# Optimization experiments

Hardware: AMD Instinct MI355X
Metric: run time of the kernel (lower is better)

## Reference

```python
import jax, jax.numpy as jnp
import numpy as np

DIM = 256
QK = 256
HEADS = 8
NWIN = 16
TOPK = 4
MLP_RATIO = 4
SCALE = QK ** -0.5


def setup_inputs() -> dict:
    key = jax.random.key(0)
    ks = jax.random.split(key, 8)
    p = lambda k, shp: jax.random.normal(k, shp, jnp.float32) * 0.02
    hid = MLP_RATIO * DIM
    return {
        "x": jax.random.normal(ks[0], (8, DIM, 64, 64), jnp.float32),
        # to_q / to_kv : 1x1 Conv2d_BN (eval-mode BN with running stats 0/1 -> scale+shift)
        "wq": p(ks[1], (QK, DIM)), "gq": jnp.ones((QK,), jnp.float32), "bq": jnp.zeros((QK,), jnp.float32),
        "wkv": p(ks[2], (QK + DIM, DIM)), "gkv": jnp.ones((QK + DIM,), jnp.float32), "bkv": jnp.zeros((QK + DIM,), jnp.float32),
        # LEPE depthwise 5x5 conv
        "w_lepe": p(ks[3], (DIM, 1, 5, 5)), "b_lepe": jnp.zeros((DIM,), jnp.float32),
        # Mlp: fc1(1x1 Conv2d_BN) -> dwconv3x3 -> ReLU -> fc2(1x1 Conv2d_BN)
        "w_fc1": p(ks[4], (hid, DIM)), "g_fc1": jnp.ones((hid,), jnp.float32), "b_fc1": jnp.zeros((hid,), jnp.float32),
        "w_dw": p(ks[5], (hid, 1, 3, 3)), "b_dw": jnp.zeros((hid,), jnp.float32),
        "w_fc2": p(ks[6], (DIM, hid)), "g_fc2": jnp.ones((DIM,), jnp.float32), "b_fc2": jnp.zeros((DIM,), jnp.float32),
    }


def _dwconv(x, w, b, pad):
    # x: NCHW, w: (C,1,k,k) depthwise
    out = jax.lax.conv_general_dilated(
        x, w, (1, 1), [(pad, pad), (pad, pad)],
        feature_group_count=x.shape[1],
        dimension_numbers=("NCHW", "OIHW", "NCHW"))
    return out + b[None, :, None, None]


def _bra(x, wq, gq, bq, wkv, gkv, bkv, w_lepe, b_lepe):
    # Bi-Level Routing Attention. x: NCHW
    N, C, H, W = x.shape
    j = i = NWIN
    h, w_ = H // j, W // i          # per-window spatial (4,4)
    p2, w2 = j * i, h * w_          # 256 windows, 16 tokens/window
    xh = x.transpose(0, 2, 3, 1)    # NHWC
    # windowize: (N, p2, h, w, C)
    xw = xh.reshape(N, j, h, i, w_, C).transpose(0, 1, 3, 2, 4, 5).reshape(N, p2, h, w_, C)
    # 1x1 conv + BN(eval: stats 0/1) == matmul * gamma + beta
    q = (xw @ wq.T) * gq + bq                    # (N,p2,h,w,QK)
    kv = (xw @ wkv.T) * gkv + bkv                # (N,p2,h,w,QK+C)
    q_pix = q.reshape(N, p2, w2, QK)
    kv_pix = kv.reshape(N, p2, w2, QK + C)       # identity kv_down
    q_win = q.mean((2, 3))                       # (N,p2,QK)
    k_win = kv[..., :QK].mean((2, 3))            # (N,p2,QK)
    # LEPE on V in full-image layout
    v_img = kv[..., QK:].reshape(N, j, i, h, w_, C).transpose(0, 1, 3, 2, 4, 5).reshape(N, H, W, C)
    lepe = _dwconv(v_img.transpose(0, 3, 1, 2), w_lepe, b_lepe, 2).transpose(0, 2, 3, 1)  # NHWC
    # window-level topk routing (detached, non-differentiable)
    qd = jax.lax.stop_gradient(q_win)
    kd = jax.lax.stop_gradient(k_win)
    logit = (qd * SCALE) @ kd.transpose(0, 2, 1)            # (N,p2,p2)
    _, r_idx = jax.lax.top_k(logit, TOPK)                   # (N,p2,TOPK); r_weight unused (mul_weight='none')
    # gather selected KV windows: (N,p2,TOPK,w2,QK+C)
    kv_sel = jax.vmap(lambda kvp, idx: kvp[idx])(kv_pix, r_idx)
    ch_k, ch_v = QK // HEADS, C // HEADS
    k_sel = kv_sel[..., :QK].reshape(N, p2, TOPK * w2, HEADS, ch_k).transpose(0, 1, 3, 2, 4)
    v_sel = kv_sel[..., QK:].reshape(N, p2, TOPK * w2, HEADS, ch_v).transpose(0, 1, 3, 2, 4)
    qh = q_pix.reshape(N, p2, w2, HEADS, ch_k).transpose(0, 1, 3, 2, 4)
    attn = jax.nn.softmax(jnp.einsum("npmqc,npmkc->npmqk", qh * SCALE, k_sel), axis=-1)
    out = jnp.einsum("npmqk,npmkc->npmqc", attn, v_sel)     # (N,p2,HEADS,w2,ch_v)
    out = out.transpose(0, 1, 3, 2, 4).reshape(N, j, i, h, w_, C)
    out = out.transpose(0, 1, 3, 2, 4, 5).reshape(N, H, W, C)
    out = out + lepe                                         # wo = Identity
    return out.transpose(0, 3, 1, 2)                         # NCHW


def reference(x, wq, gq, bq, wkv, gkv, bkv, w_lepe, b_lepe,
              w_fc1, g_fc1, b_fc1, w_dw, b_dw, w_fc2, g_fc2, b_fc2):
    # top_Block: x = x + attn(x); x = x + mlp(x)   (drop_path inactive in eval)
    x = x + _bra(x, wq, gq, bq, wkv, gkv, bkv, w_lepe, b_lepe)
    h1 = jnp.einsum("nchw,dc->ndhw", x, w_fc1) * g_fc1[None, :, None, None] + b_fc1[None, :, None, None]
    h1 = jax.nn.relu(_dwconv(h1, w_dw, b_dw, 1))
    h2 = jnp.einsum("nchw,dc->ndhw", h1, w_fc2) * g_fc2[None, :, None, None] + b_fc2[None, :, None, None]
    return x + h2
```

## Files before the change

kernel.cpp:

```cpp
#include <hip/hip_runtime.h>
#include <hip/hip_bf16.h>

#define NBATCH 8
#define CDIM 256
#define HH 64
#define WW 64
#define HWSZ 4096
#define TT 32768
#define QKVD 768
#define TOPK 4
#define HID 1024
#define ATTN_SCALE 0.0625f

typedef __hip_bfloat16 bf16;
typedef __attribute__((ext_vector_type(8))) short s8v;
typedef __attribute__((ext_vector_type(4))) float f4v;

__device__ __forceinline__ float toF(bf16 v) { return __bfloat162float(v); }
__device__ __forceinline__ bf16  toB(float v) { return __float2bfloat16(v); }

__global__ void k_prep(const float* __restrict__ wq, const float* __restrict__ gq,
                       const float* __restrict__ wkv, const float* __restrict__ gkv,
                       const float* __restrict__ wfc1, const float* __restrict__ gfc1,
                       const float* __restrict__ wfc2, const float* __restrict__ gfc2,
                       const float* __restrict__ bq, const float* __restrict__ bkv,
                       const float* __restrict__ w_dw, const float* __restrict__ b_dw,
                       bf16* __restrict__ wbqkv, bf16* __restrict__ wbfc1,
                       bf16* __restrict__ wbfc2, float* __restrict__ bias768,
                       float* __restrict__ wdwT) {
    int i = blockIdx.x * 256 + threadIdx.x;
    if (i < 196608) {
        int r = i >> 8;
        float g = (r < 256) ? gq[r] : gkv[r - 256];
        float w = (r < 256) ? wq[i] : wkv[i - 65536];
        wbqkv[i] = toB(w * g);
        if (i < 768) bias768[i] = (i < 256) ? bq[i] : bkv[i - 256];
    } else if (i < 458752) {
        int j = i - 196608;
        wbfc1[j] = toB(wfc1[j] * gfc1[j >> 8]);
    } else if (i < 720896) {
        int j = i - 458752;
        wbfc2[j] = toB(wfc2[j] * gfc2[j >> 10]);
    } else if (i < 731136) {
        int j = i - 720896;
        int cg = j / 80, r = j - cg * 80;
        wdwT[j] = (r < 72) ? w_dw[(cg * 8 + r / 9) * 9 + (r % 9)]
                           : b_dw[cg * 8 + (r - 72)];
    }
}

__global__ void k_xt(const float* __restrict__ x, bf16* __restrict__ xt) {
    __shared__ float tile[32][33];
    int s0 = blockIdx.x * 32, c0 = blockIdx.y * 32, n = blockIdx.z;
    int tx = threadIdx.x, ty = threadIdx.y;
#pragma unroll
    for (int r = 0; r < 4; r++)
        tile[ty + r * 8][tx] = x[(size_t)n * CDIM * HWSZ + (size_t)(c0 + ty + r * 8) * HWSZ + s0 + tx];
    __syncthreads();
#pragma unroll
    for (int r = 0; r < 4; r++)
        xt[((size_t)n * HWSZ + s0 + ty + r * 8) * CDIM + c0 + tx] = toB(tile[tx][ty + r * 8]);
}

__global__ void k_xwin(const float* __restrict__ x, float* __restrict__ xwin) {
    int b = blockIdx.x;
    int n = b >> 8, c = b & 255;
    int p = threadIdx.x, wy = p >> 4, wx = p & 15;
    const float* pl = x + ((size_t)n * CDIM + c) * HWSZ;
    float s = 0.f;
#pragma unroll
    for (int dy = 0; dy < 4; dy++)
#pragma unroll
        for (int dx = 0; dx < 4; dx++)
            s += pl[(wy * 4 + dy) * WW + wx * 4 + dx];
    xwin[((size_t)(n << 8) + p) * 256 + c] = s * 0.0625f;
}

__global__ void k_qkwin(const float* __restrict__ xwin,
                        const float* __restrict__ wq, const float* __restrict__ wkv,
                        const float* __restrict__ gq, const float* __restrict__ bq,
                        const float* __restrict__ gkv, const float* __restrict__ bkv,
                        float* __restrict__ qkwin) {
    __shared__ float As[16][68];
    __shared__ float Bs[16][68];
    int m0 = blockIdx.x * 64, n0 = blockIdx.y * 64;
    int tid = threadIdx.x;
    int tx = tid & 15, ty = tid >> 4;
    float acc[4][4] = {};
    for (int k0 = 0; k0 < 256; k0 += 16) {
#pragma unroll
        for (int r = 0; r < 4; r++) {
            int lin = tid + r * 256;
            int row = lin >> 4, kk = lin & 15;
            As[kk][row] = xwin[(size_t)(m0 + row) * 256 + k0 + kk];
            int n = n0 + row;
            const float* wr = (n < 256) ? (wq + (size_t)n * 256) : (wkv + (size_t)(n - 256) * 256);
            Bs[kk][row] = wr[k0 + kk];
        }
        __syncthreads();
#pragma unroll
        for (int kk = 0; kk < 16; kk++) {
            float a[4], bb[4];
#pragma unroll
            for (int i = 0; i < 4; i++) a[i] = As[kk][tx * 4 + i];
#pragma unroll
            for (int j = 0; j < 4; j++) bb[j] = Bs[kk][ty * 4 + j];
#pragma unroll
            for (int i = 0; i < 4; i++)
#pragma unroll
                for (int j = 0; j < 4; j++) acc[i][j] += a[i] * bb[j];
        }
        __syncthreads();
    }
#pragma unroll
    for (int j = 0; j < 4; j++) {
        int n = n0 + ty * 4 + j;
        float gg = (n < 256) ? gq[n] : gkv[n - 256];
        float bb = (n < 256) ? bq[n] : bkv[n - 256];
#pragma unroll
        for (int i = 0; i < 4; i++)
            qkwin[(size_t)(m0 + tx * 4 + i) * 512 + n] = acc[i][j] * gg + bb;
    }
}

__global__ void k_route(const float* __restrict__ qkwin, int* __restrict__ topk) {
    __shared__ float qrow[256];
    __shared__ float vals[256];
    __shared__ float rv[256];
    __shared__ int ri[256];
    int b = blockIdx.x;
    int n = b >> 8, pq = b & 255;
    int tid = threadIdx.x;
    qrow[tid] = qkwin[((size_t)(n << 8) + pq) * 512 + tid];
    __syncthreads();
    const float* krow = qkwin + ((size_t)(n << 8) + tid) * 512 + 256;
    float dot = 0.f;
    for (int o = 0; o < 256; o++) dot += qrow[o] * krow[o];
    vals[tid] = dot;
    __syncthreads();
    for (int sel = 0; sel < TOPK; sel++) {
        rv[tid] = vals[tid];
        ri[tid] = tid;
        __syncthreads();
        for (int off = 128; off > 0; off >>= 1) {
            if (tid < off) {
                if (rv[tid + off] > rv[tid] ||
                    (rv[tid + off] == rv[tid] && ri[tid + off] < ri[tid])) {
                    rv[tid] = rv[tid + off];
                    ri[tid] = ri[tid + off];
                }
            }
            __syncthreads();
        }
        if (tid == 0) {
            topk[((size_t)(n << 8) + pq) * TOPK + sel] = ri[0];
            vals[ri[0]] = -INFINITY;
        }
        __syncthreads();
    }
}

template <int BM, int BN, int OUTMODE>
__global__ __launch_bounds__(256) void k_mfma(const bf16* __restrict__ A,
                                              const bf16* __restrict__ Wb,
                                              const float* __restrict__ bias,
                                              bf16* __restrict__ out,
                                              bf16* __restrict__ out2,
                                              int M, int N, int K) {
    constexpr int WROWS = BM / 2, WCOLS = BN / 2;
    constexpr int WM = WROWS / 16, WN = WCOLS / 16;
    constexpr int CA = (BM * 4) / 256;
    constexpr int CB = (BN * 4) / 256;
    __shared__ bf16 As[BM * 32];
    __shared__ bf16 Bs[BN * 32];
    int m0 = blockIdx.x * BM, n0 = blockIdx.y * BN;
    int tid = threadIdx.x;
    int w = tid >> 6, lane = tid & 63;
    int wr = w >> 1, wc = w & 1;
    int lm = lane & 15, lq = lane >> 4;
    f4v acc[WM][WN];
#pragma unroll
    for (int i = 0; i < WM; i++)
#pragma unroll
        for (int j = 0; j < WN; j++) acc[i][j] = (f4v){0.f, 0.f, 0.f, 0.f};

    for (int k0 = 0; k0 < K; k0 += 32) {
        s8v va[CA], vb[CB];
#pragma unroll
        for (int q = 0; q < CA; q++) {
            int c = tid + q * 256, row = c >> 2, col = c & 3;
            va[q] = *(const s8v*)(A + (size_t)(m0 + row) * K + k0 + col * 8);
        }
#pragma unroll
        for (int q = 0; q < CB; q++) {
            int c = tid + q * 256, row = c >> 2, col = c & 3;
            vb[q] = *(const s8v*)(Wb + (size_t)(n0 + row) * K + k0 + col * 8);
        }
        __syncthreads();
#pragma unroll
        for (int q = 0; q < CA; q++) {
            int c = tid + q * 256, row = c >> 2, col = c & 3;
            *(s8v*)&As[row * 32 + col * 8] = va[q];
        }
#pragma unroll
        for (int q = 0; q < CB; q++) {
            int c = tid + q * 256, row = c >> 2, col = c & 3;
            *(s8v*)&Bs[row * 32 + col * 8] = vb[q];
        }
        __syncthreads();
        s8v af[WM], bfr[WN];
#pragma unroll
        for (int i = 0; i < WM; i++)
            af[i] = *(const s8v*)&As[(wr * WROWS + i * 16 + lm) * 32 + lq * 8];
#pragma unroll
        for (int j = 0; j < WN; j++)
            bfr[j] = *(const s8v*)&Bs[(wc * WCOLS + j * 16 + lm) * 32 + lq * 8];
#pragma unroll
        for (int i = 0; i < WM; i++)
#pragma unroll
            for (int j = 0; j < WN; j++)
                acc[i][j] = __builtin_amdgcn_mfma_f32_16x16x32_bf16(af[i], bfr[j], acc[i][j], 0, 0, 0);
    }
#pragma unroll
    for (int j = 0; j < WN; j++) {
        int n = n0 + wc * WCOLS + j * 16 + lm;
        float bb = bias[n];
#pragma unroll
        for (int i = 0; i < WM; i++) {
            int mb = m0 + wr * WROWS + i * 16 + lq * 4;
#pragma unroll
            for (int r = 0; r < 4; r++)
                out[(size_t)(mb + r) * N + n] = toB(acc[i][j][r] + bb);
            if (OUTMODE == 1 && n >= 512) {
                bf16* dst = out2 + ((size_t)(mb >> 12) * CDIM + (n - 512)) * HWSZ + (mb & 4095);
#pragma unroll
                for (int r = 0; r < 4; r++) dst[r] = toB(acc[i][j][r] + bb);
            }
        }
    }
}

__global__ void k_lepe_pl(bf16* __restrict__ vpl, const float* __restrict__ w_lepe,
                          const float* __restrict__ b_lepe) {
    __shared__ float pl[HWSZ];
    int b = blockIdx.x;
    int n = b >> 8, c = b & 255;
    int tid = threadIdx.x;
    bf16* plane = vpl + ((size_t)n * CDIM + c) * HWSZ;
#pragma unroll
    for (int k = 0; k < 16; k++) pl[tid + k * 256] = toF(plane[tid + k * 256]);
    float wreg[25];
#pragma unroll
    for (int i = 0; i < 25; i++) wreg[i] = w_lepe[c * 25 + i];
    float bias = b_lepe[c];
    __syncthreads();
#pragma unroll
    for (int k = 0; k < 16; k++) {
        int s = tid + k * 256;
        int y = s >> 6, xx0 = s & 63;
        float acc = bias;
#pragma unroll
        for (int dy = -2; dy <= 2; dy++) {
            int yy = y + dy;
            if (yy < 0 || yy >= HH) continue;
#pragma unroll
            for (int dx = -2; dx <= 2; dx++) {
                int xx = xx0 + dx;
                if (xx < 0 || xx >= WW) continue;
                acc += pl[yy * 64 + xx] * wreg[(dy + 2) * 5 + (dx + 2)];
            }
        }
        plane[s] = toB(acc);
    }
}

__global__ __launch_bounds__(256) void k_attn(const bf16* __restrict__ qkv,
                                              const int* __restrict__ topk,
                                              bf16* __restrict__ attnout) {
    __shared__ bf16 vst[256][72];
    __shared__ bf16 plds[4][16][72];
    __shared__ float lsm[4][16];
    __shared__ int toks[64];
    int b = blockIdx.x;
    int n = b >> 8, p = b & 255;
    int wy = p >> 4, wx = p & 15;
    int tid = threadIdx.x;
    if (tid < 64) {
        int rp = topk[((size_t)(n << 8) + p) * TOPK + (tid >> 4)] & 255;
        int st = tid & 15;
        toks[tid] = ((rp >> 4) * 4 + (st >> 2)) * WW + (rp & 15) * 4 + (st & 3);
    }
    __syncthreads();
    const bf16* qbase = qkv + (size_t)n * HWSZ * QKVD;
    {
        int kt = tid & 63, jj = tid >> 6;
#pragma unroll
        for (int pass = 0; pass < 8; pass++) {
            int d0 = pass * 32 + jj * 8;
            uint4 v = *(const uint4*)(qbase + (size_t)toks[kt] * QKVD + 512 + d0);
            const bf16* pv = (const bf16*)&v;
#pragma unroll
            for (int e = 0; e < 8; e++) vst[d0 + e][kt] = pv[e];
        }
    }
    __syncthreads();
    int w = tid >> 6, lane = tid & 63;
    int ln = lane & 15, lq = lane >> 4;
    int myS = (wy * 4 + (ln >> 2)) * WW + wx * 4 + (ln & 3);
    const f4v fz = {0.f, 0.f, 0.f, 0.f};
    for (int hh = 0; hh < 2; hh++) {
        int h = w * 2 + hh;
        s8v qf = *(const s8v*)(qbase + (size_t)myS * QKVD + h * 32 + lq * 8);
        f4v st4[4];
#pragma unroll
        for (int t = 0; t < 4; t++) {
            s8v kf = *(const s8v*)(qbase + (size_t)toks[t * 16 + ln] * QKVD + 256 + h * 32 + lq * 8);
            st4[t] = __builtin_amdgcn_mfma_f32_16x16x32_bf16(kf, qf, fz, 0, 0, 0);
        }
        float mx = -INFINITY;
#pragma unroll
        for (int t = 0; t < 4; t++)
#pragma unroll
            for (int r = 0; r < 4; r++) mx = fmaxf(mx, st4[t][r]);
        mx = fmaxf(mx, __shfl_xor(mx, 16));
        mx = fmaxf(mx, __shfl_xor(mx, 32));
        mx *= ATTN_SCALE;
        float sum = 0.f;
#pragma unroll
        for (int t = 0; t < 4; t++)
#pragma unroll
            for (int r = 0; r < 4; r++) {
                float pp = __expf(st4[t][r] * ATTN_SCALE - mx);
                sum += pp;
                plds[w][ln][t * 16 + lq * 4 + r] = toB(pp);
            }
        sum += __shfl_xor(sum, 16);
        sum += __shfl_xor(sum, 32);
        if (lq == 0) lsm[w][ln] = sum;
        __syncthreads();
        s8v ap0 = *(const s8v*)&plds[w][ln][lq * 8];
        s8v ap1 = *(const s8v*)&plds[w][ln][32 + lq * 8];
#pragma unroll
        for (int dt = 0; dt < 2; dt++) {
            int dim = h * 32 + dt * 16 + ln;
            s8v vv0 = *(const s8v*)&vst[dim][lq * 8];
            s8v vv1 = *(const s8v*)&vst[dim][32 + lq * 8];
            f4v o = __builtin_amdgcn_mfma_f32_16x16x32_bf16(ap0, vv0, fz, 0, 0, 0);
            o = __builtin_amdgcn_mfma_f32_16x16x32_bf16(ap1, vv1, o, 0, 0, 0);
#pragma unroll
            for (int r = 0; r < 4; r++) {
                int t = lq * 4 + r;
                float linv = 1.f / lsm[w][t];
                int s = (wy * 4 + (t >> 2)) * WW + wx * 4 + (t & 3);
                attnout[((size_t)n * HWSZ + s) * CDIM + dim] = toB(o[r] * linv);
            }
        }
        __syncthreads();
    }
}

__global__ void k_x1(const bf16* __restrict__ xt, const bf16* __restrict__ lepe,
                     const bf16* __restrict__ attnout, bf16* __restrict__ x1) {
    __shared__ float tile[32][33];
    int s0 = blockIdx.x * 32, c0 = blockIdx.y * 32, n = blockIdx.z;
    int tx = threadIdx.x, ty = threadIdx.y;
#pragma unroll
    for (int r = 0; r < 4; r++) {
        int c = c0 + ty + r * 8;
        tile[ty + r * 8][tx] = toF(lepe[((size_t)n * CDIM + c) * HWSZ + s0 + tx]);
    }
    __syncthreads();
#pragma unroll
    for (int r = 0; r < 4; r++) {
        int s = s0 + ty + r * 8;
        size_t idx = ((size_t)n * HWSZ + s) * CDIM + c0 + tx;
        x1[idx] = toB(toF(xt[idx]) + toF(attnout[idx]) + tile[tx][ty + r * 8]);
    }
}

__global__ __launch_bounds__(256) void k_dw3_t(const bf16* __restrict__ h1,
                                               const float* __restrict__ wdwT,
                                               bf16* __restrict__ h1p) {
    int tid = threadIdx.x;
    int cg = tid & 127;
    int slot = tid >> 7;
    int seg = blockIdx.x;
    int img = blockIdx.y;
    int y = seg >> 2;
    int x0 = ((seg & 3) << 4) + (slot << 3);
    const float* wp = wdwT + cg * 80;
    float w[72], bias[8];
#pragma unroll
    for (int i = 0; i < 72; i++) w[i] = wp[i];
#pragma unroll
    for (int c = 0; c < 8; c++) bias[c] = wp[72 + c];
    const uint4* src = (const uint4*)h1 + (size_t)img * HWSZ * 128;
    uint4* dst = (uint4*)h1p + (size_t)img * HWSZ * 128;
#pragma unroll
    for (int xi = 0; xi < 8; xi++) {
        int x = x0 + xi;
        float o[8];
#pragma unroll
        for (int c = 0; c < 8; c++) o[c] = bias[c];
#pragma unroll
        for (int dy = -1; dy <= 1; dy++) {
            int yy = y + dy;
            if (yy < 0 || yy >= HH) continue;
#pragma unroll
            for (int dx = -1; dx <= 1; dx++) {
                int xx = x + dx;
                if (xx < 0 || xx >= WW) continue;
                int k = (dy + 1) * 3 + (dx + 1);
                uint4 v = src[(size_t)(yy * WW + xx) * 128 + cg];
                const bf16* pv = (const bf16*)&v;
#pragma unroll
                for (int c = 0; c < 8; c++) o[c] += toF(pv[c]) * w[c * 9 + k];
            }
        }
        uint4 pk;
        bf16* pb = (bf16*)&pk;
#pragma unroll
        for (int c = 0; c < 8; c++) pb[c] = toB(fmaxf(o[c], 0.f));
        dst[(size_t)(y * WW + x) * 128 + cg] = pk;
    }
}

__global__ void k_final(const bf16* __restrict__ x1, const bf16* __restrict__ h2,
                        float* __restrict__ out) {
    __shared__ float tile[32][33];
    int s0 = blockIdx.x * 32, c0 = blockIdx.y * 32, n = blockIdx.z;
    int tx = threadIdx.x, ty = threadIdx.y;
#pragma unroll
    for (int r = 0; r < 4; r++) {
        int s = s0 + ty + r * 8;
        size_t idx = ((size_t)n * HWSZ + s) * CDIM + c0 + tx;
        tile[tx][ty + r * 8] = toF(x1[idx]) + toF(h2[idx]);
    }
    __syncthreads();
#pragma unroll
    for (int r = 0; r < 4; r++) {
        int c = c0 + ty + r * 8;
        out[(size_t)n * CDIM * HWSZ + (size_t)c * HWSZ + s0 + tx] = tile[ty + r * 8][tx];
    }
}

extern "C" void kernel_launch(void* const* d_in, const int* in_sizes, int n_in,
                              void* d_out, int out_size, void* d_ws, size_t ws_size,
                              hipStream_t stream) {
    (void)in_sizes; (void)n_in; (void)out_size; (void)ws_size;
    const float* x      = (const float*)d_in[0];
    const float* wq     = (const float*)d_in[1];
    const float* gq     = (const float*)d_in[2];
    const float* bq     = (const float*)d_in[3];
    const float* wkv    = (const float*)d_in[4];
    const float* gkv    = (const float*)d_in[5];
    const float* bkv    = (const float*)d_in[6];
    const float* w_lepe = (const float*)d_in[7];
    const float* b_lepe = (const float*)d_in[8];
    const float* w_fc1  = (const float*)d_in[9];
    const float* g_fc1  = (const float*)d_in[10];
    const float* b_fc1  = (const float*)d_in[11];
    const float* w_dw   = (const float*)d_in[12];
    const float* b_dw   = (const float*)d_in[13];
    const float* w_fc2  = (const float*)d_in[14];
    const float* g_fc2  = (const float*)d_in[15];
    const float* b_fc2  = (const float*)d_in[16];

    char* ws = (char*)d_ws;
    bf16*  qkv    = (bf16*)(ws);
    bf16*  vpl    = (bf16*)(ws + 50331648);
    bf16*  attn   = (bf16*)(ws + 67108864);
    bf16*  xt     = (bf16*)(ws + 83886080);
    bf16*  x1     = (bf16*)(ws + 83886080);
    bf16*  h1     = (bf16*)(ws);
    bf16*  h1p    = (bf16*)(ws + 33554432);
    bf16*  h2     = (bf16*)(ws + 67108864);
    float* xwin   = (float*)(ws + 100663296);
    float* qkwin  = (float*)(ws + 102760448);
    int*   tk     = (int*)(ws + 106954752);
    bf16*  wbqkv  = (bf16*)(ws + 106987520);
    bf16*  wbfc1  = (bf16*)(ws + 107380736);
    bf16*  wbfc2  = (bf16*)(ws + 107905024);
    float* bias768= (float*)(ws + 108429312);
    float* wdwT   = (float*)(ws + 108433408);

    k_prep<<<2856, 256, 0, stream>>>(wq, gq, wkv, gkv, w_fc1, g_fc1, w_fc2, g_fc2,
                                     bq, bkv, w_dw, b_dw,
                                     wbqkv, wbfc1, wbfc2, bias768, wdwT);
    k_xt<<<dim3(128, 8, 8), dim3(32, 8), 0, stream>>>(x, xt);
    k_xwin<<<2048, 256, 0, stream>>>(x, xwin);
    k_qkwin<<<dim3(32, 8), 256, 0, stream>>>(xwin, wq, wkv, gq, bq, gkv, bkv, qkwin);
    k_route<<<2048, 256, 0, stream>>>(qkwin, tk);
    k_mfma<128, 128, 1><<<dim3(256, 6), 256, 0, stream>>>(
        xt, wbqkv, bias768, qkv, vpl, TT, QKVD, CDIM);
    k_lepe_pl<<<2048, 256, 0, stream>>>(vpl, w_lepe, b_lepe);
    k_attn<<<2048, 256, 0, stream>>>(qkv, tk, attn);
    k_x1<<<dim3(128, 8, 8), dim3(32, 8), 0, stream>>>(xt, vpl, attn, x1);
    for (int c = 0; c < 2; c++) {
        bf16* x1c = x1 + (size_t)c * 16384 * CDIM;
        bf16* h2c = h2 + (size_t)c * 16384 * CDIM;
        k_mfma<128, 128, 0><<<dim3(128, 8), 256, 0, stream>>>(
            x1c, wbfc1, b_fc1, h1, nullptr, 16384, HID, CDIM);
        k_dw3_t<<<dim3(256, 4), 256, 0, stream>>>(h1, wdwT, h1p);
        k_mfma<64, 128, 0><<<dim3(256, 2), 256, 0, stream>>>(
            h1p, wbfc2, b_fc2, h2c, nullptr, 16384, CDIM, HID);
    }
    k_final<<<dim3(128, 8, 8), dim3(32, 8), 0, stream>>>(x1, h2, (float*)d_out);
}
```

Baseline: 463.9 us.

## Split routing into tiled logits GEMM and wavefront-shuffle top-k kernel

The per-query routing kernel, which had every thread read a full 256-element key row from global memory, becomes two kernels. The first is a shared-memory tiled 64x64 GEMM per image that computes all window-to-window logits into a workspace buffer. The second is a top-k pass in which one 64-lane wavefront per row uses xor shuffles instead of repeated shared-memory tree reductions with barriers. This removes redundant global reads and many syncthreads calls, at the cost of one extra launch and a logits round trip through global memory.

```diff
diff --git a/kernel.cpp b/kernel.cpp
--- a/kernel.cpp
+++ b/kernel.cpp
@@ -123,40 +123,65 @@
     }
 }
 
-__global__ void k_route(const float* __restrict__ qkwin, int* __restrict__ topk) {
-    __shared__ float qrow[256];
-    __shared__ float vals[256];
-    __shared__ float rv[256];
-    __shared__ int ri[256];
-    int b = blockIdx.x;
-    int n = b >> 8, pq = b & 255;
+__global__ void k_logits(const float* __restrict__ qkwin, float* __restrict__ logits) {
+    __shared__ float As[16][68];
+    __shared__ float Bs[16][68];
+    int m0 = blockIdx.x * 64, n0 = blockIdx.y * 64, img = blockIdx.z;
+    const float* base = qkwin + (size_t)(img << 8) * 512;
     int tid = threadIdx.x;
-    qrow[tid] = qkwin[((size_t)(n << 8) + pq) * 512 + tid];
-    __syncthreads();
-    const float* krow = qkwin + ((size_t)(n << 8) + tid) * 512 + 256;
-    float dot = 0.f;
-    for (int o = 0; o < 256; o++) dot += qrow[o] * krow[o];
-    vals[tid] = dot;
-    __syncthreads();
+    int tx = tid & 15, ty = tid >> 4;
+    float acc[4][4] = {};
+    for (int k0 = 0; k0 < 256; k0 += 16) {
+#pragma unroll
+        for (int r = 0; r < 4; r++) {
+            int lin = tid + r * 256;
+            int row = lin >> 4, kk = lin & 15;
+            As[kk][row] = base[(size_t)(m0 + row) * 512 + k0 + kk];
+            Bs[kk][row] = base[(size_t)(n0 + row) * 512 + 256 + k0 + kk];
+        }
+        __syncthreads();
+#pragma unroll
+        for (int kk = 0; kk < 16; kk++) {
+            float a[4], bb[4];
+#pragma unroll
+            for (int i = 0; i < 4; i++) a[i] = As[kk][tx * 4 + i];
+#pragma unroll
+            for (int j = 0; j < 4; j++) bb[j] = Bs[kk][ty * 4 + j];
+#pragma unroll
+            for (int i = 0; i < 4; i++)
+#pragma unroll
+                for (int j = 0; j < 4; j++) acc[i][j] += a[i] * bb[j];
+        }
+        __syncthreads();
+    }
+    float* Lr = logits + (size_t)(img << 8) * 256;
+#pragma unroll
+    for (int j = 0; j < 4; j++)
+#pragma unroll
+        for (int i = 0; i < 4; i++)
+            Lr[(size_t)(m0 + tx * 4 + i) * 256 + n0 + ty * 4 + j] = acc[i][j];
+}
+
+__global__ __launch_bounds__(256) void k_topk(const float* __restrict__ logits,
+                                              int* __restrict__ topk) {
+    int row = blockIdx.x * 4 + (threadIdx.x >> 6);
+    int lane = threadIdx.x & 63;
+    float4 v4 = *(const float4*)(logits + (size_t)row * 256 + lane * 4);
+    float v[4] = {v4.x, v4.y, v4.z, v4.w};
+#pragma unroll
     for (int sel = 0; sel < TOPK; sel++) {
-        rv[tid] = vals[tid];
-        ri[tid] = tid;
-        __syncthreads();
-        for (int off = 128; off > 0; off >>= 1) {
-            if (tid < off) {
-                if (rv[tid + off] > rv[tid] ||
-                    (rv[tid + off] == rv[tid] && ri[tid + off] < ri[tid])) {
-                    rv[tid] = rv[tid + off];
-                    ri[tid] = ri[tid + off];
-                }
-            }
-            __syncthreads();
-        }
-        if (tid == 0) {
-            topk[((size_t)(n << 8) + pq) * TOPK + sel] = ri[0];
-            vals[ri[0]] = -INFINITY;
-        }
-        __syncthreads();
+        float mv = v[0]; int mi = lane * 4;
+#pragma unroll
+        for (int j = 1; j < 4; j++)
+            if (v[j] > mv) { mv = v[j]; mi = lane * 4 + j; }
+#pragma unroll
+        for (int off = 1; off < 64; off <<= 1) {
+            float ov = __shfl_xor(mv, off);
+            int oi = __shfl_xor(mi, off);
+            if (ov > mv || (ov == mv && oi < mi)) { mv = ov; mi = oi; }
+        }
+        if (lane == 0) topk[(size_t)row * TOPK + sel] = mi;
+        if ((mi >> 2) == lane) v[mi & 3] = -INFINITY;
     }
 }
 
@@ -483,6 +508,7 @@
     bf16*  wbfc2  = (bf16*)(ws + 107905024);
     float* bias768= (float*)(ws + 108429312);
     float* wdwT   = (float*)(ws + 108433408);
+    float* logits = (float*)(ws + 108478464);
 
     k_prep<<<2856, 256, 0, stream>>>(wq, gq, wkv, gkv, w_fc1, g_fc1, w_fc2, g_fc2,
                                      bq, bkv, w_dw, b_dw,
@@ -490,7 +516,8 @@
     k_xt<<<dim3(128, 8, 8), dim3(32, 8), 0, stream>>>(x, xt);
     k_xwin<<<2048, 256, 0, stream>>>(x, xwin);
     k_qkwin<<<dim3(32, 8), 256, 0, stream>>>(xwin, wq, wkv, gq, bq, gkv, bkv, qkwin);
-    k_route<<<2048, 256, 0, stream>>>(qkwin, tk);
+    k_logits<<<dim3(4, 4, 8), 256, 0, stream>>>(qkwin, logits);
+    k_topk<<<512, 256, 0, stream>>>(logits, tk);
     k_mfma<128, 128, 1><<<dim3(256, 6), 256, 0, stream>>>(
         xt, wbqkv, bias768, qkv, vpl, TT, QKVD, CDIM);
     k_lepe_pl<<<2048, 256, 0, stream>>>(vpl, w_lepe, b_lepe);
```

Result: faster. 425.0 us (-8.4%).
